# Kernel tuning notes

Measured on AMD Instinct MI355X. Metric: run time of the kernel, lower is better.

Reference implementation:

```python
import jax, jax.numpy as jnp
from jax import lax
import numpy as np
import math

B = 8
DIFF_LEN, HORIZON, NUM_NODES = 336, 96, 1024
SEG_LEN, D_CONV, D_MODEL = 8, 64, 128
NUM_KERNELS, DEPTH, ALPHA = 6, 2, 0.05
FREQ = math.ceil(DIFF_LEN / SEG_LEN)      # 42
STEP = math.ceil(HORIZON / SEG_LEN)       # 12
PAD = SEG_LEN * FREQ - DIFF_LEN           # 0 here, code stays general
MAXK = 2 * NUM_KERNELS - 1                # 11


def setup_inputs() -> dict:
    key = jax.random.key(0)
    ks = iter(jax.random.split(key, 64))
    p = lambda *s: 0.02 * jax.random.normal(next(ks), s, jnp.float32)
    inp = dict(
        x_diff=jax.random.normal(next(ks), (B, DIFF_LEN, NUM_NODES), jnp.float32),
        adj=jax.random.uniform(next(ks), (NUM_NODES, NUM_NODES), jnp.float32),
        enc_w1=p(SEG_LEN, D_MODEL), enc_b1=p(D_MODEL),
        enc_w2=p(D_MODEL, D_CONV), enc_b2=p(D_CONV),
        dec_w1=p(D_CONV, D_MODEL), dec_b1=p(D_MODEL),
        dec_w2=p(D_MODEL, SEG_LEN), dec_b2=p(SEG_LEN),
        g1_w=p((DEPTH + 1) * D_CONV, D_CONV), g1_b=p(D_CONV),
        g2_w=p((DEPTH + 1) * D_CONV, D_CONV), g2_b=p(D_CONV),
    )
    for i in range(NUM_KERNELS):
        inp[f'conv_w{i}'] = p(D_CONV, D_CONV, 1, 2 * i + 1)
        inp[f'conv_b{i}'] = p(D_CONV)
    return inp


def _mlp(x, w1, b1, w2, b2):
    # 2-hidden-layer MLP with ReLU (dropout = identity at eval)
    return jnp.maximum(x @ w1 + b1, 0.0) @ w2 + b2


def _t_inception(x, conv_ws, conv_bs):
    # x: (B, D, N, T); inception = mean of 'same'-padded (1, 2i+1) convs
    out = jnp.zeros_like(x)
    for i, (w, b) in enumerate(zip(conv_ws, conv_bs)):
        out = out + lax.conv_general_dilated(
            x, w, (1, 1), ((0, 0), (i, i)),
            dimension_numbers=('NCHW', 'OIHW', 'NCHW')) + b[None, :, None, None]
    return out / len(conv_ws)


def _norm_adj(adj):
    a = adj + jnp.eye(adj.shape[0], dtype=adj.dtype)
    return a / a.sum(1, keepdims=True)


def _mixprop(x, a, w, b):
    # x: (B, T, N, D), a: row-normalized (N, N)
    h = x
    outs = [h]
    for _ in range(DEPTH):
        h = ALPHA * x + (1.0 - ALPHA) * jnp.einsum('vn,btnd->btvd', a, h)
        outs.append(h)
    return jnp.concatenate(outs, -1) @ w + b


def _stconv(x, a1, a2, conv_ws, conv_bs, g1_w, g1_b, g2_w, g2_b):
    res = jnp.transpose(x, (0, 3, 2, 1))            # b d n t
    res = _t_inception(res, conv_ws, conv_bs)
    res = jnp.transpose(res, (0, 3, 2, 1))          # b t n d
    res = _mixprop(res, a1, g1_w, g1_b) + _mixprop(res, a2, g2_w, g2_b)
    return res + x                                   # dropout = identity at eval


def reference(x_diff, adj,
              enc_w1, enc_b1, enc_w2, enc_b2,
              dec_w1, dec_b1, dec_w2, dec_b2,
              g1_w, g1_b, g2_w, g2_b,
              conv_w0, conv_b0, conv_w1, conv_b1, conv_w2, conv_b2,
              conv_w3, conv_b3, conv_w4, conv_b4, conv_w5, conv_b5):
    conv_ws = [conv_w0, conv_w1, conv_w2, conv_w3, conv_w4, conv_w5]
    conv_bs = [conv_b0, conv_b1, conv_b2, conv_b3, conv_b4, conv_b5]
    Bb, L, N = x_diff.shape
    a1 = _norm_adj(adj)
    a2 = _norm_adj(adj.T)

    # segment + left-pad with tail so length = FREQ * SEG_LEN
    res = jnp.concatenate((x_diff[:, L - PAD:, :], x_diff), axis=1)
    res = res.reshape(Bb, FREQ, SEG_LEN, N)
    res = jnp.transpose(res, (0, 1, 3, 2))          # (B, F, N, P)
    res = _mlp(res, enc_w1, enc_b1, enc_w2, enc_b2)  # (B, F, N, D)

    # reconstruction branch (teacher-forced one-step shift)
    rec = jnp.concatenate(
        (res[:, :1],
         _stconv(res[:, :-1], a1, a2, conv_ws, conv_bs, g1_w, g1_b, g2_w, g2_b)),
        axis=1)
    rec = _mlp(rec, dec_w1, dec_b1, dec_w2, dec_b2)  # (B, F, N, P)
    rec = jnp.transpose(rec, (0, 1, 3, 2)).reshape(Bb, FREQ * SEG_LEN, N)
    rec = rec[:, -DIFF_LEN:, :]

    cur = res[:, -MAXK:]                             # (B, MAXK, N, D)
    preds = []
    for _ in range(STEP):
        p = _stconv(cur, a1, a2, conv_ws, conv_bs, g1_w, g1_b, g2_w, g2_b)[:, -1:]
        preds.append(p)
        cur = jnp.concatenate((cur[:, 1:], p), axis=1)
    pred = jnp.concatenate(preds, axis=1)            # (B, STEP, N, D)
    pred = _mlp(pred, dec_w1, dec_b1, dec_w2, dec_b2)  # (B, STEP, N, SEG)
    # NOTE: original torch code does a raw .reshape (not transpose); replicate it
    pred = pred.reshape(Bb, STEP * SEG_LEN, N)[:, :HORIZON, :]
    return (rec, pred)
```

## Files before the change

kernel.cpp:

```cpp
#include <hip/hip_runtime.h>

typedef __bf16 bf16;
typedef __bf16 bf16x8 __attribute__((ext_vector_type(8)));
typedef float f32x4 __attribute__((ext_vector_type(4)));

#define N_NODES 1024
#define DC 64
#define FREQ 42
#define TREC 41
#define NB 8
#define MAXK 11
#define NSTEP 12
#define SLICE 65536

__global__ void transpose_k(const float* __restrict__ in, float* __restrict__ out) {
  __shared__ float tile[32][33];
  int bx = blockIdx.x * 32, by = blockIdx.y * 32;
  int x = threadIdx.x, y = threadIdx.y;
#pragma unroll
  for (int j = 0; j < 32; j += 8) tile[y + j][x] = in[(size_t)(by + y + j) * N_NODES + bx + x];
  __syncthreads();
#pragma unroll
  for (int j = 0; j < 32; j += 8) out[(size_t)(bx + y + j) * N_NODES + by + x] = tile[x][y + j];
}

__global__ void rowsum_k(const float* __restrict__ m, float* __restrict__ sums) {
  int v = blockIdx.x;
  float s = 0.f;
  for (int n = threadIdx.x; n < N_NODES; n += 256) s += m[(size_t)v * N_NODES + n];
  __shared__ float red[256];
  red[threadIdx.x] = s;
  __syncthreads();
  for (int w = 128; w > 0; w >>= 1) {
    if (threadIdx.x < w) red[threadIdx.x] += red[threadIdx.x + w];
    __syncthreads();
  }
  if (threadIdx.x == 0) sums[v] = red[0] + 1.0f;
}

__global__ void norm_k(const float* __restrict__ adj, const float* __restrict__ adjT,
                       const float* __restrict__ rs, const float* __restrict__ cs,
                       bf16* __restrict__ a1, bf16* __restrict__ a2) {
  int v = blockIdx.x & (N_NODES - 1);
  bool second = blockIdx.x >= N_NODES;
  const float* src = second ? adjT : adj;
  float inv = 1.0f / (second ? cs[v] : rs[v]);
  bf16* dst = second ? a2 : a1;
  for (int n = threadIdx.x; n < N_NODES; n += 256) {
    float val = src[(size_t)v * N_NODES + n] + (n == v ? 1.0f : 0.0f);
    dst[(size_t)v * N_NODES + n] = (bf16)(val * inv);
  }
}

__global__ __launch_bounds__(256) void btrans_k(const bf16* __restrict__ src,
                                                bf16* __restrict__ dst) {
  __shared__ __align__(16) bf16 t[64][72];
  int bx = blockIdx.x * 64, by = blockIdx.y * 64;
  int tid = threadIdx.x;
#pragma unroll
  for (int i = 0; i < 2; ++i) {
    int q = tid + i * 256;
    int r = q >> 3, c = (q & 7) * 8;
    *(uint4*)&t[r][c] = *(const uint4*)&src[(size_t)(by + r) * N_NODES + bx + c];
  }
  __syncthreads();
#pragma unroll
  for (int i = 0; i < 2; ++i) {
    int q = tid + i * 256;
    int rr = q >> 3, cc = (q & 7) * 8;
    bf16 tmp[8];
#pragma unroll
    for (int e = 0; e < 8; ++e) tmp[e] = t[cc + e][rr];
    *(uint4*)&dst[(size_t)(bx + rr) * N_NODES + by + cc] = *(uint4*)tmp;
  }
}

__global__ void combine_w_k(const float* w0, const float* w1, const float* w2, const float* w3,
                            const float* w4, const float* w5, const float* b0, const float* b1,
                            const float* b2, const float* b3, const float* b4, const float* b5,
                            bf16* __restrict__ Wc, float* __restrict__ bsum) {
  int idx = blockIdx.x * 256 + threadIdx.x;
  if (idx < MAXK * 4096) {
    int dtI = idx >> 12;
    int dout = (idx >> 6) & 63;
    int di = idx & 63;
    int d = dtI - 5;
    int ad = d < 0 ? -d : d;
    const float* ws[6] = {w0, w1, w2, w3, w4, w5};
    float s = 0.f;
    for (int i = 0; i < 6; ++i)
      if (i >= ad) {
        int K = 2 * i + 1;
        s += ws[i][((size_t)dout * 64 + di) * K + (d + i)];
      }
    Wc[idx] = (bf16)s;
  }
  if (idx < 64) bsum[idx] = b0[idx] + b1[idx] + b2[idx] + b3[idx] + b4[idx] + b5[idx];
}

__global__ void vt_k(const float* __restrict__ g1w, const float* __restrict__ g2w,
                     const float* __restrict__ g1b, const float* __restrict__ g2b,
                     bf16* __restrict__ Vt, float* __restrict__ gbsum) {
  int idx = blockIdx.x * 256 + threadIdx.x;
  if (idx < 64) gbsum[idx] = g1b[idx] + g2b[idx];
  if (idx >= 5 * 4096) return;
  int j = idx >> 12;
  int dout = (idx >> 6) & 63;
  int din = idx & 63;
  const float al = 0.05f, bt = 0.95f;
  float v;
  if (j == 0)
    v = g1w[din * 64 + dout] + g2w[din * 64 + dout] +
        al * (g1w[(64 + din) * 64 + dout] + g1w[(128 + din) * 64 + dout] +
              g2w[(64 + din) * 64 + dout] + g2w[(128 + din) * 64 + dout]);
  else if (j == 1)
    v = bt * g1w[(64 + din) * 64 + dout] + al * bt * g1w[(128 + din) * 64 + dout];
  else if (j == 2)
    v = bt * bt * g1w[(128 + din) * 64 + dout];
  else if (j == 3)
    v = bt * g2w[(64 + din) * 64 + dout] + al * bt * g2w[(128 + din) * 64 + dout];
  else
    v = bt * bt * g2w[(128 + din) * 64 + dout];
  Vt[idx] = (bf16)v;
}

__global__ void prep_misc_k(const float* __restrict__ w2, const float* __restrict__ dw1,
                            const float* __restrict__ dw2, bf16* __restrict__ w2T,
                            bf16* __restrict__ dw1T, bf16* __restrict__ dw2T) {
  int i = blockIdx.x * 256 + threadIdx.x;
  if (i < 8192) {
    int dout = i >> 7, j = i & 127;
    w2T[i] = (bf16)w2[(size_t)j * 64 + dout];
    int jj = i >> 6, k = i & 63;
    dw1T[i] = (bf16)dw1[k * 128 + jj];
  }
  if (i < 2048) {
    int s = i >> 7, j = i & 127;
    dw2T[i] = (s < 8) ? (bf16)dw2[j * 8 + s] : (bf16)0.f;
  }
}

__global__ __launch_bounds__(256) void encoder_k(const float* __restrict__ x,
                                                 const float* __restrict__ w1,
                                                 const float* __restrict__ b1,
                                                 const bf16* __restrict__ w2T,
                                                 const float* __restrict__ b2,
                                                 bf16* __restrict__ resb) {
  __shared__ __align__(16) float xs[8 * 64];
  __shared__ __align__(16) float w1s[8 * 128];
  __shared__ float b1s[128];
  __shared__ float b2s[64];
  __shared__ __align__(16) bf16 hA[64 * 136];
  __shared__ __align__(16) bf16 wB[64 * 136];
  int tid = threadIdx.x;
  int v0 = blockIdx.x * 64;
  int bfp = blockIdx.y;
  int b = bfp / FREQ, f = bfp % FREQ;
#pragma unroll
  for (int i = 0; i < 2; ++i) {
    int q = tid + i * 256;
    xs[q] = x[(size_t)(b * 336 + f * 8 + (q >> 6)) * 1024 + v0 + (q & 63)];
  }
#pragma unroll
  for (int i = 0; i < 4; ++i) {
    int q = tid + i * 256;
    w1s[q] = w1[q];
  }
#pragma unroll
  for (int i = 0; i < 4; ++i) {
    int q = tid + i * 256;
    int dout = q >> 4, jc = (q & 15) * 8;
    *(uint4*)&wB[dout * 136 + jc] = *(const uint4*)&w2T[dout * 128 + jc];
  }
  if (tid < 128) b1s[tid] = b1[tid];
  if (tid < 64) b2s[tid] = b2[tid];
  __syncthreads();
  {
    int n = tid & 63, jc = (tid >> 6) * 32;
    for (int jj = 0; jj < 32; ++jj) {
      int j = jc + jj;
      float a = b1s[j];
#pragma unroll
      for (int k = 0; k < 8; ++k) a = fmaf(xs[k * 64 + n], w1s[k * 128 + j], a);
      hA[n * 136 + j] = (bf16)fmaxf(a, 0.f);
    }
  }
  __syncthreads();
  int wid = tid >> 6, lane = tid & 63, lr = lane & 15, lg = lane >> 4;
  f32x4 acc[4] = {};
#pragma unroll
  for (int ks = 0; ks < 4; ++ks) {
    bf16x8 a = *(const bf16x8*)&hA[(wid * 16 + lr) * 136 + ks * 32 + lg * 8];
#pragma unroll
    for (int ni = 0; ni < 4; ++ni) {
      bf16x8 bb = *(const bf16x8*)&wB[(ni * 16 + lr) * 136 + ks * 32 + lg * 8];
      acc[ni] = __builtin_amdgcn_mfma_f32_16x16x32_bf16(a, bb, acc[ni], 0, 0, 0);
    }
  }
  __syncthreads();
#pragma unroll
  for (int ni = 0; ni < 4; ++ni) {
    int n = ni * 16 + lr;
    float bz = b2s[n];
#pragma unroll
    for (int r = 0; r < 4; ++r) wB[(wid * 16 + lg * 4 + r) * 72 + n] = (bf16)(acc[ni][r] + bz);
  }
  __syncthreads();
  size_t so = (size_t)(b * FREQ + f) * SLICE;
#pragma unroll
  for (int i = 0; i < 2; ++i) {
    int q = tid + i * 256;
    int r = q >> 3, c = (q & 7) * 8;
    *(uint4*)&resb[so + (size_t)(v0 + r) * 64 + c] = *(uint4*)&wB[r * 72 + c];
  }
}

__global__ void curinit_k(const bf16* __restrict__ resb, float* __restrict__ cur,
                          bf16* __restrict__ curb) {
  size_t idx = (size_t)blockIdx.x * 256 + threadIdx.x;
  const size_t per_b = (size_t)MAXK * SLICE;
  if (idx < (size_t)NB * per_b) {
    size_t b = idx / per_b, rem = idx % per_b;
    bf16 v = resb[b * ((size_t)FREQ * SLICE) + (size_t)31 * SLICE + rem];
    cur[idx] = (float)v;
    curb[idx] = v;
  }
}

__device__ __forceinline__ void stageA(bf16* lds_a, const bf16* src, int rowStride, int tid) {
#pragma unroll
  for (int i = 0; i < 8; ++i) {
    int q = tid + i * 256;
    int r = q >> 3, c = (q & 7) << 3;
    *(uint4*)&lds_a[r * 72 + c] = *(const uint4*)&src[(size_t)r * rowStride + c];
  }
}
__device__ __forceinline__ void stageB(bf16* lds_b, const bf16* src, int rowStride, int tid) {
#pragma unroll
  for (int i = 0; i < 2; ++i) {
    int q = tid + i * 256;
    int r = q >> 3, c = (q & 7) << 3;
    *(uint4*)&lds_b[r * 72 + c] = *(const uint4*)&src[(size_t)r * rowStride + c];
  }
}
__device__ __forceinline__ void mfma64(const bf16* lds_a, const bf16* lds_b, int wid, int lane,
                                       f32x4 acc[4][4]) {
  int lr = lane & 15, lg = lane >> 4;
#pragma unroll
  for (int h = 0; h < 2; ++h) {
    bf16x8 af[4], bfr[4];
#pragma unroll
    for (int mi = 0; mi < 4; ++mi)
      af[mi] = *(const bf16x8*)&lds_a[(wid * 64 + mi * 16 + lr) * 72 + h * 32 + lg * 8];
#pragma unroll
    for (int ni = 0; ni < 4; ++ni)
      bfr[ni] = *(const bf16x8*)&lds_b[(ni * 16 + lr) * 72 + h * 32 + lg * 8];
#pragma unroll
    for (int mi = 0; mi < 4; ++mi)
#pragma unroll
      for (int ni = 0; ni < 4; ++ni)
        acc[mi][ni] =
            __builtin_amdgcn_mfma_f32_16x16x32_bf16(af[mi], bfr[ni], acc[mi][ni], 0, 0, 0);
  }
}

__global__ __launch_bounds__(256) void asq_k(const bf16* __restrict__ a,
                                             const bf16* __restrict__ aT,
                                             bf16* __restrict__ out) {
  __shared__ __align__(16) bf16 As[64 * 72];
  __shared__ __align__(16) bf16 Bs2[64 * 72];
  int tid = threadIdx.x, w = tid >> 6, lane = tid & 63;
  int lr = lane & 15, lg = lane >> 4;
  int v0 = blockIdx.x * 64, n0 = blockIdx.y * 64;
  f32x4 acc[4] = {};
  for (int k0 = 0; k0 < 1024; k0 += 64) {
    __syncthreads();
    stageB(As, a + (size_t)v0 * 1024 + k0, 1024, tid);
    stageB(Bs2, aT + (size_t)n0 * 1024 + k0, 1024, tid);
    __syncthreads();
#pragma unroll
    for (int h = 0; h < 2; ++h) {
      bf16x8 av = *(const bf16x8*)&As[(w * 16 + lr) * 72 + h * 32 + lg * 8];
#pragma unroll
      for (int ni = 0; ni < 4; ++ni) {
        bf16x8 bv = *(const bf16x8*)&Bs2[(ni * 16 + lr) * 72 + h * 32 + lg * 8];
        acc[ni] = __builtin_amdgcn_mfma_f32_16x16x32_bf16(av, bv, acc[ni], 0, 0, 0);
      }
    }
  }
#pragma unroll
  for (int ni = 0; ni < 4; ++ni)
#pragma unroll
    for (int r = 0; r < 4; ++r) As[(w * 16 + lg * 4 + r) * 72 + ni * 16 + lr] = (bf16)acc[ni][r];
  __syncthreads();
#pragma unroll
  for (int i = 0; i < 2; ++i) {
    int q = tid + i * 256;
    int r = q >> 3, c = (q & 7) * 8;
    *(uint4*)&out[(size_t)(v0 + r) * 1024 + n0 + c] = *(uint4*)&As[r * 72 + c];
  }
}

__global__ __launch_bounds__(256) void incep_k(const bf16* __restrict__ resb, int b0,
                                               const bf16* __restrict__ Wc,
                                               const float* __restrict__ bsum,
                                               bf16* __restrict__ xcN, bf16* __restrict__ xcF) {
  __shared__ __align__(16) bf16 lds_a[256 * 72];
  __shared__ __align__(16) bf16 lds_b[64 * 72];
  int tid = threadIdx.x, wid = tid >> 6, lane = tid & 63;
  int v0 = blockIdx.x * 256;
  int sl = blockIdx.y;
  int b = b0 + sl / TREC, tt = sl % TREC;
  f32x4 acc[4][4] = {};
  for (int dt = 0; dt < MAXK; ++dt) {
    int ts = tt + dt - 5;
    if (ts < 0 || ts >= TREC) continue;
    __syncthreads();
    stageA(lds_a, resb + (size_t)(b * FREQ + ts) * SLICE + (size_t)v0 * 64, 64, tid);
    stageB(lds_b, Wc + dt * 4096, 64, tid);
    __syncthreads();
    mfma64(lds_a, lds_b, wid, lane, acc);
  }
  int lr = lane & 15, lg = lane >> 4;
  size_t so = (size_t)sl * SLICE;
  __syncthreads();
#pragma unroll
  for (int mi = 0; mi < 4; ++mi)
#pragma unroll
    for (int ni = 0; ni < 4; ++ni) {
      int n = ni * 16 + lr;
      float bs = bsum[n];
      union { bf16 h[4]; uint2 u; } pk;
#pragma unroll
      for (int r = 0; r < 4; ++r) {
        int m = wid * 64 + mi * 16 + lg * 4 + r;
        bf16 bv = (bf16)((acc[mi][ni][r] + bs) * (1.f / 6.f));
        lds_a[m * 72 + n] = bv;
        pk.h[r] = bv;
      }
      *(uint2*)&xcF[so + (size_t)n * 1024 + v0 + wid * 64 + mi * 16 + lg * 4] = pk.u;
    }
  __syncthreads();
#pragma unroll
  for (int i = 0; i < 8; ++i) {
    int q = tid + i * 256;
    int r = q >> 3, c = (q & 7) * 8;
    *(uint4*)&xcN[so + (size_t)(v0 + r) * 64 + c] = *(uint4*)&lds_a[r * 72 + c];
  }
}

__global__ __launch_bounds__(256) void fusedrec_k(
    const bf16* __restrict__ xcN, const bf16* __restrict__ xcF, const bf16* __restrict__ a1,
    const bf16* __restrict__ a1q, const bf16* __restrict__ a2, const bf16* __restrict__ a2q,
    const bf16* __restrict__ Vt, const float* __restrict__ gbsum,
    const bf16* __restrict__ resb, int b0, const bf16* __restrict__ dw1T,
    const float* __restrict__ db1, const bf16* __restrict__ dw2T,
    const float* __restrict__ db2, float* __restrict__ outRec) {
  __shared__ __align__(16) bf16 reg1[4][64 * 72];
  __shared__ __align__(16) bf16 reg2[64 * 72];
  __shared__ __align__(16) bf16 valb[64 * 72];
  bf16* hb = &reg1[0][0];
  int tid = threadIdx.x, w = tid >> 6, lane = tid & 63;
  int lr = lane & 15, lg = lane >> 4;
  int v0 = blockIdx.x * 64;
  int sy = blockIdx.y;
  int bl = sy / FREQ, f = sy % FREQ;
  int b = b0 + bl;

  if (f == 0) {
    const bf16* src = resb + (size_t)(b * FREQ) * SLICE + (size_t)v0 * 64;
#pragma unroll
    for (int i = 0; i < 2; ++i) {
      int q = tid + i * 256;
      int r = q >> 3, c = (q & 7) * 8;
      *(uint4*)&valb[r * 72 + c] = *(const uint4*)&src[(size_t)r * 64 + c];
    }
    __syncthreads();
  } else {
    int tt = f - 1;
    size_t so = (size_t)(bl * TREC + tt) * SLICE;
    f32x4 acc[4][4] = {};
    for (int k0 = 0; k0 < 1024; k0 += 64) {
      __syncthreads();
#pragma unroll
      for (int i = 0; i < 8; ++i) {
        int q = tid + i * 256;
        int mm = q >> 9, pos = q & 511;
        int rr = pos >> 3, cc = (pos & 7) * 8;
        const bf16* mp = mm == 0 ? a1 : (mm == 1 ? a1q : (mm == 2 ? a2 : a2q));
        *(uint4*)&reg1[mm][rr * 72 + cc] = *(const uint4*)&mp[(size_t)(v0 + rr) * 1024 + k0 + cc];
      }
#pragma unroll
      for (int i = 0; i < 2; ++i) {
        int q = tid + i * 256;
        int rb = q >> 3, cbb = (q & 7) * 8;
        *(uint4*)&reg2[rb * 72 + cbb] = *(const uint4*)&xcF[so + (size_t)rb * 1024 + k0 + cbb];
      }
      __syncthreads();
#pragma unroll
      for (int h = 0; h < 2; ++h) {
        bf16x8 af[4], bfr[4];
#pragma unroll
        for (int mi = 0; mi < 4; ++mi)
          af[mi] = *(const bf16x8*)&reg1[w][(mi * 16 + lr) * 72 + h * 32 + lg * 8];
#pragma unroll
        for (int ni = 0; ni < 4; ++ni)
          bfr[ni] = *(const bf16x8*)&reg2[(ni * 16 + lr) * 72 + h * 32 + lg * 8];
#pragma unroll
        for (int mi = 0; mi < 4; ++mi)
#pragma unroll
          for (int ni = 0; ni < 4; ++ni)
            acc[mi][ni] =
                __builtin_amdgcn_mfma_f32_16x16x32_bf16(af[mi], bfr[ni], acc[mi][ni], 0, 0, 0);
      }
    }
    __syncthreads();
#pragma unroll
    for (int mi = 0; mi < 4; ++mi)
#pragma unroll
      for (int ni = 0; ni < 4; ++ni)
#pragma unroll
        for (int r = 0; r < 4; ++r)
          reg1[w][(mi * 16 + lg * 4 + r) * 72 + ni * 16 + lr] = (bf16)acc[mi][ni][r];
#pragma unroll
    for (int i = 0; i < 2; ++i) {
      int q = tid + i * 256;
      int r = q >> 3, c = (q & 7) * 8;
      *(uint4*)&reg2[r * 72 + c] = *(const uint4*)&xcN[so + (size_t)(v0 + r) * 64 + c];
    }
    __syncthreads();
    f32x4 z[4] = {};
#pragma unroll
    for (int j = 0; j < 5; ++j) {
      const bf16* Asrc = (j == 0) ? reg2 : &reg1[j - 1][0];
#pragma unroll
      for (int h = 0; h < 2; ++h) {
        bf16x8 a = *(const bf16x8*)&Asrc[(w * 16 + lr) * 72 + h * 32 + lg * 8];
#pragma unroll
        for (int ni = 0; ni < 4; ++ni) {
          bf16x8 bb =
              *(const bf16x8*)&Vt[(size_t)j * 4096 + (ni * 16 + lr) * 64 + h * 32 + lg * 8];
          z[ni] = __builtin_amdgcn_mfma_f32_16x16x32_bf16(a, bb, z[ni], 0, 0, 0);
        }
      }
    }
    const bf16* xb = resb + (size_t)(b * FREQ + tt) * SLICE + (size_t)v0 * 64;
#pragma unroll
    for (int ni = 0; ni < 4; ++ni) {
      int n = ni * 16 + lr;
      float gb = gbsum[n];
#pragma unroll
      for (int r = 0; r < 4; ++r) {
        int m = w * 16 + lg * 4 + r;
        valb[m * 72 + n] = (bf16)((float)xb[(size_t)m * 64 + n] + z[ni][r] + gb);
      }
    }
    __syncthreads();
  }
  f32x4 hacc[4][2] = {};
#pragma unroll
  for (int h = 0; h < 2; ++h) {
    bf16x8 a[4];
#pragma unroll
    for (int mi = 0; mi < 4; ++mi)
      a[mi] = *(const bf16x8*)&valb[(mi * 16 + lr) * 72 + h * 32 + lg * 8];
#pragma unroll
    for (int ni2 = 0; ni2 < 2; ++ni2) {
      bf16x8 bb = *(const bf16x8*)&dw1T[(w * 32 + ni2 * 16 + lr) * 64 + h * 32 + lg * 8];
#pragma unroll
      for (int mi = 0; mi < 4; ++mi)
        hacc[mi][ni2] = __builtin_amdgcn_mfma_f32_16x16x32_bf16(a[mi], bb, hacc[mi][ni2], 0, 0, 0);
    }
  }
  __syncthreads();
#pragma unroll
  for (int ni2 = 0; ni2 < 2; ++ni2) {
    int j = w * 32 + ni2 * 16 + lr;
    float bz = db1[j];
#pragma unroll
    for (int mi = 0; mi < 4; ++mi)
#pragma unroll
      for (int r = 0; r < 4; ++r)
        hb[(mi * 16 + lg * 4 + r) * 136 + j] = (bf16)fmaxf(hacc[mi][ni2][r] + bz, 0.f);
  }
  __syncthreads();
  f32x4 oacc = {};
#pragma unroll
  for (int kc = 0; kc < 4; ++kc) {
    bf16x8 a = *(const bf16x8*)&hb[(w * 16 + lr) * 136 + kc * 32 + lg * 8];
    bf16x8 bb = *(const bf16x8*)&dw2T[lr * 128 + kc * 32 + lg * 8];
    oacc = __builtin_amdgcn_mfma_f32_16x16x32_bf16(a, bb, oacc, 0, 0, 0);
  }
  if (lr < 8) {
    float bz = db2[lr];
    float4 o;
    o.x = oacc[0] + bz;
    o.y = oacc[1] + bz;
    o.z = oacc[2] + bz;
    o.w = oacc[3] + bz;
    *(float4*)&outRec[(size_t)b * 344064 + (size_t)(f * 8 + lr) * 1024 + v0 + w * 16 + lg * 4] =
        o;
  }
}

__device__ __forceinline__ void arrive_wait(unsigned* c, int tid) {
  __syncthreads();
  if (tid == 0) {
    __hip_atomic_fetch_add(c, 1u, __ATOMIC_RELAXED, __HIP_MEMORY_SCOPE_AGENT);
    while (__hip_atomic_load(c, __ATOMIC_RELAXED, __HIP_MEMORY_SCOPE_AGENT) < 64u)
      __builtin_amdgcn_s_sleep(8);
  }
  __syncthreads();
}

__device__ __forceinline__ void incep16(const bf16* __restrict__ curb,
                                        const bf16* __restrict__ Wc, const float* bsums_,
                                        int base, int b, int r0, int w, int lr, int lg,
                                        bf16* yL, bf16* yFdst) {
  f32x4 ya = {};
  for (int j = 0; j < 6; ++j) {
    int slot = (base + 5 + j) % MAXK;
    const bf16* cb = curb + ((size_t)b * MAXK + slot) * SLICE + (size_t)r0 * 64;
#pragma unroll
    for (int h = 0; h < 2; ++h) {
      bf16x8 a = *(const bf16x8*)&cb[lr * 64 + h * 32 + lg * 8];
      bf16x8 bb = *(const bf16x8*)&Wc[(size_t)j * 4096 + (w * 16 + lr) * 64 + h * 32 + lg * 8];
      ya = __builtin_amdgcn_mfma_f32_16x16x32_bf16(a, bb, ya, 0, 0, 0);
    }
  }
  int n = w * 16 + lr;
  float bs = bsums_[n];
  union { bf16 h[4]; unsigned long long u; } pk;
#pragma unroll
  for (int r = 0; r < 4; ++r) {
    int m = lg * 4 + r;
    bf16 bv = (bf16)((ya[r] + bs) * (1.f / 6.f));
    yL[m * 72 + n] = bv;
    pk.h[r] = bv;
  }
  __hip_atomic_store((unsigned long long*)(yFdst + (size_t)n * 1024 + r0 + lg * 4), pk.u,
                     __ATOMIC_RELAXED, __HIP_MEMORY_SCOPE_AGENT);
}

struct AR5 {
  const bf16 *Wc;
  const float *bsum;
  const bf16 *a1, *a1q, *a2, *a2q;
  const bf16 *Vt;
  const float *gbsum;
  float *cur;
  bf16 *curb;
  bf16 *yF;
  const bf16 *dw1T;
  const float *db1;
  const bf16 *dw2T;
  const float *db2;
  float *outPred;
  unsigned *bar;
};

__global__ void __launch_bounds__(256) ar6_k(AR5 p) {
  __shared__ __align__(16) bf16 As4[2][4][16 * 72];
  __shared__ __align__(16) bf16 Bs[2][64 * 72];
  __shared__ __align__(16) bf16 yL[16 * 72];
  __shared__ __align__(16) bf16 PL[4][16 * 72];
  __shared__ __align__(16) bf16 valb[16 * 72];
  __shared__ __align__(16) bf16 hb[16 * 136];
  __shared__ float db1s[128], db2s[8], bsums[64], gbsums[64];
  int tid = threadIdx.x, w = tid >> 6, lane = tid & 63;
  int lr = lane & 15, lg = lane >> 4;
  int bid = blockIdx.x, b = bid >> 6, l = bid & 63;
  unsigned* cnt = p.bar + b * 32;
  int r0 = l * 16;

  if (tid < 128) db1s[tid] = p.db1[tid];
  if (tid < 8) db2s[tid] = p.db2[tid];
  if (tid < 64) {
    bsums[tid] = p.bsum[tid];
    gbsums[tid] = p.gbsum[tid];
  }
  __syncthreads();

  incep16(p.curb, p.Wc, bsums, 0, b, r0, w, lr, lg, yL, p.yF + (size_t)b * SLICE);
  arrive_wait(cnt + 0, tid);

  const bf16* mats[4] = {p.a1, p.a1q, p.a2, p.a2q};
  for (int s = 0; s < NSTEP; ++s) {
    {
      const bf16* yFs = p.yF + ((size_t)s * NB + b) * SLICE;
      f32x4 acc[4] = {};
      auto stage_chunk = [&](int d, int k0) {
#pragma unroll
        for (int i = 0; i < 2; ++i) {
          int q = tid + i * 256;
          int mm = q >> 7, rr = (q >> 3) & 15, cc = (q & 7) * 8;
          *(uint4*)&As4[d][mm][rr * 72 + cc] =
              *(const uint4*)&mats[mm][(size_t)(r0 + rr) * 1024 + k0 + cc];
          int rb = q >> 3, cb2 = (q & 7) * 8;
          *(uint4*)&Bs[d][rb * 72 + cb2] = *(const uint4*)&yFs[(size_t)rb * 1024 + k0 + cb2];
        }
      };
      stage_chunk(0, 0);
      for (int c = 0; c < 16; ++c) {
        __syncthreads();
        if (c < 15) stage_chunk((c + 1) & 1, (c + 1) * 64);
#pragma unroll
        for (int h = 0; h < 2; ++h) {
          bf16x8 a = *(const bf16x8*)&As4[c & 1][w][lr * 72 + h * 32 + lg * 8];
#pragma unroll
          for (int ni = 0; ni < 4; ++ni) {
            bf16x8 bb = *(const bf16x8*)&Bs[c & 1][(ni * 16 + lr) * 72 + h * 32 + lg * 8];
            acc[ni] = __builtin_amdgcn_mfma_f32_16x16x32_bf16(a, bb, acc[ni], 0, 0, 0);
          }
        }
      }
#pragma unroll
      for (int ni = 0; ni < 4; ++ni) {
        int nn = ni * 16 + lr;
#pragma unroll
        for (int r = 0; r < 4; ++r) PL[w][(lg * 4 + r) * 72 + nn] = (bf16)acc[ni][r];
      }
    }
    __syncthreads();
    {
      f32x4 z = {};
#pragma unroll
      for (int j = 0; j < 5; ++j) {
        const bf16* Aj = (j == 0) ? yL : PL[j - 1];
#pragma unroll
        for (int h = 0; h < 2; ++h) {
          bf16x8 a = *(const bf16x8*)&Aj[lr * 72 + h * 32 + lg * 8];
          bf16x8 bb =
              *(const bf16x8*)&p.Vt[(size_t)j * 4096 + (w * 16 + lr) * 64 + h * 32 + lg * 8];
          z = __builtin_amdgcn_mfma_f32_16x16x32_bf16(a, bb, z, 0, 0, 0);
        }
      }
      int slotR = (s + 10) % MAXK, slotW = s % MAXK;
      size_t xo = ((size_t)b * MAXK + slotR) * SLICE + (size_t)r0 * 64;
      size_t wo = ((size_t)b * MAXK + slotW) * SLICE + (size_t)r0 * 64;
      int n = w * 16 + lr;
      float gb = gbsums[n];
#pragma unroll
      for (int r = 0; r < 4; ++r) {
        int m = lg * 4 + r;
        size_t o = (size_t)m * 64 + n;
        float v = p.cur[xo + o] + z[r] + gb;
        p.cur[wo + o] = v;
        p.curb[wo + o] = (bf16)v;
        valb[m * 72 + n] = (bf16)v;
      }
      __syncthreads();
      if (s < NSTEP - 1)
        incep16(p.curb, p.Wc, bsums, s + 1, b, r0, w, lr, lg, yL,
                p.yF + ((size_t)(s + 1) * NB + b) * SLICE);
      f32x4 hacc[2] = {};
#pragma unroll
      for (int h = 0; h < 2; ++h) {
        bf16x8 a = *(const bf16x8*)&valb[lr * 72 + h * 32 + lg * 8];
#pragma unroll
        for (int ni2 = 0; ni2 < 2; ++ni2) {
          bf16x8 bb = *(const bf16x8*)&p.dw1T[(w * 32 + ni2 * 16 + lr) * 64 + h * 32 + lg * 8];
          hacc[ni2] = __builtin_amdgcn_mfma_f32_16x16x32_bf16(a, bb, hacc[ni2], 0, 0, 0);
        }
      }
#pragma unroll
      for (int ni2 = 0; ni2 < 2; ++ni2) {
        int j = w * 32 + ni2 * 16 + lr;
        float bz = db1s[j];
#pragma unroll
        for (int r = 0; r < 4; ++r)
          hb[(lg * 4 + r) * 136 + j] = (bf16)fmaxf(hacc[ni2][r] + bz, 0.f);
      }
      __syncthreads();
      f32x4 oacc = {};
#pragma unroll
      for (int kc = 0; kc < 4; ++kc) {
        bf16x8 a = *(const bf16x8*)&hb[lr * 136 + kc * 32 + lg * 8];
        bf16x8 bb = *(const bf16x8*)&p.dw2T[lr * 128 + kc * 32 + lg * 8];
        oacc = __builtin_amdgcn_mfma_f32_16x16x32_bf16(a, bb, oacc, 0, 0, 0);
      }
      if (w == 0 && lr < 8) {
        float bz = db2s[lr];
#pragma unroll
        for (int r = 0; r < 4; ++r)
          p.outPred[(size_t)b * 98304 + (size_t)s * 8192 + (size_t)(r0 + lg * 4 + r) * 8 + lr] =
              oacc[r] + bz;
      }
    }
    if (s < NSTEP - 1) arrive_wait(cnt + 1 + s, tid);
  }
}

extern "C" void kernel_launch(void* const* d_in, const int* in_sizes, int n_in, void* d_out,
                              int out_size, void* d_ws, size_t ws_size, hipStream_t stream) {
  const float* x_diff = (const float*)d_in[0];
  const float* adj = (const float*)d_in[1];
  const float* enc_w1 = (const float*)d_in[2];
  const float* enc_b1 = (const float*)d_in[3];
  const float* enc_w2 = (const float*)d_in[4];
  const float* enc_b2 = (const float*)d_in[5];
  const float* dec_w1 = (const float*)d_in[6];
  const float* dec_b1 = (const float*)d_in[7];
  const float* dec_w2 = (const float*)d_in[8];
  const float* dec_b2 = (const float*)d_in[9];
  const float* g1_w = (const float*)d_in[10];
  const float* g1_b = (const float*)d_in[11];
  const float* g2_w = (const float*)d_in[12];
  const float* g2_b = (const float*)d_in[13];
  const float* cw[6];
  const float* cb_[6];
  for (int i = 0; i < 6; ++i) {
    cw[i] = (const float*)d_in[14 + 2 * i];
    cb_[i] = (const float*)d_in[15 + 2 * i];
  }

  char* base = (char*)d_ws;
  size_t off = 0;
  auto alloc = [&](size_t bytes) -> void* {
    void* p = base + off;
    off = (off + bytes + 255) & ~(size_t)255;
    return p;
  };
  float* adjT = (float*)alloc(1048576ULL * 4);
  float* rowsum = (float*)alloc(4096);
  float* colsum = (float*)alloc(4096);
  bf16* a1b = (bf16*)alloc(1048576ULL * 2);
  bf16* a2b = (bf16*)alloc(1048576ULL * 2);
  bf16* a1T = (bf16*)alloc(1048576ULL * 2);
  bf16* a2T = (bf16*)alloc(1048576ULL * 2);
  bf16* a1q = (bf16*)alloc(1048576ULL * 2);
  bf16* a2q = (bf16*)alloc(1048576ULL * 2);
  bf16* Wc = (bf16*)alloc(45056ULL * 2);
  float* bsum = (float*)alloc(256);
  float* gbsum = (float*)alloc(256);
  bf16* Vt = (bf16*)alloc(20480ULL * 2);
  bf16* w2T = (bf16*)alloc(8192ULL * 2);
  bf16* dw1T = (bf16*)alloc(8192ULL * 2);
  bf16* dw2T = (bf16*)alloc(2048ULL * 2);
  bf16* resb = (bf16*)alloc((size_t)NB * FREQ * SLICE * 2);
  float* cur = (float*)alloc((size_t)NB * MAXK * SLICE * 4);
  bf16* curb = (bf16*)alloc((size_t)NB * MAXK * SLICE * 2);
  bf16* yF = (bf16*)alloc((size_t)NSTEP * NB * SLICE * 2);
  unsigned* gbar = (unsigned*)alloc(4096);
  size_t fixedEnd = off;
  int cb = NB;
  while (cb > 1) {
    size_t S = (size_t)TREC * cb;
    if (fixedEnd + S * SLICE * 4 + 65536 <= ws_size) break;
    cb >>= 1;
  }
  size_t S = (size_t)TREC * cb;
  bf16* xcN = (bf16*)alloc(S * SLICE * 2);
  bf16* xcF = (bf16*)alloc(S * SLICE * 2);

  float* outF = (float*)d_out;
  float* outRec = outF;
  float* outPred = outF + (size_t)2752512;

  transpose_k<<<dim3(32, 32), dim3(32, 8), 0, stream>>>(adj, adjT);
  rowsum_k<<<1024, 256, 0, stream>>>(adj, rowsum);
  rowsum_k<<<1024, 256, 0, stream>>>(adjT, colsum);
  norm_k<<<2048, 256, 0, stream>>>(adj, adjT, rowsum, colsum, a1b, a2b);
  btrans_k<<<dim3(16, 16), 256, 0, stream>>>(a1b, a1T);
  btrans_k<<<dim3(16, 16), 256, 0, stream>>>(a2b, a2T);
  asq_k<<<dim3(16, 16), 256, 0, stream>>>(a1b, a1T, a1q);
  asq_k<<<dim3(16, 16), 256, 0, stream>>>(a2b, a2T, a2q);
  combine_w_k<<<(MAXK * 4096 + 255) / 256, 256, 0, stream>>>(cw[0], cw[1], cw[2], cw[3], cw[4],
                                                             cw[5], cb_[0], cb_[1], cb_[2],
                                                             cb_[3], cb_[4], cb_[5], Wc, bsum);
  vt_k<<<80, 256, 0, stream>>>(g1_w, g2_w, g1_b, g2_b, Vt, gbsum);
  prep_misc_k<<<32, 256, 0, stream>>>(enc_w2, dec_w1, dec_w2, w2T, dw1T, dw2T);
  encoder_k<<<dim3(16, NB * FREQ), 256, 0, stream>>>(x_diff, enc_w1, enc_b1, w2T, enc_b2,
                                                     resb);
  curinit_k<<<(int)(((size_t)NB * MAXK * SLICE + 255) / 256), 256, 0, stream>>>(resb, cur,
                                                                                curb);

  for (int c0 = 0; c0 < NB; c0 += cb) {
    int Sg = TREC * cb;
    incep_k<<<dim3(4, Sg), 256, 0, stream>>>(resb, c0, Wc, bsum, xcN, xcF);
    fusedrec_k<<<dim3(16, cb * FREQ), 256, 0, stream>>>(xcN, xcF, a1b, a1q, a2b, a2q, Vt,
                                                        gbsum, resb, c0, dw1T, dec_b1, dw2T,
                                                        dec_b2, outRec);
  }

  hipMemsetAsync(gbar, 0, 4096, stream);
  AR5 arp;
  arp.Wc = Wc; arp.bsum = bsum;
  arp.a1 = a1b; arp.a1q = a1q; arp.a2 = a2b; arp.a2q = a2q;
  arp.Vt = Vt; arp.gbsum = gbsum;
  arp.cur = cur; arp.curb = curb;
  arp.yF = yF;
  arp.dw1T = dw1T; arp.db1 = dec_b1; arp.dw2T = dw2T; arp.db2 = dec_b2;
  arp.outPred = outPred;
  arp.bar = gbar;
  ar6_k<<<dim3(512), dim3(256), 0, stream>>>(arp);
}
```

Baseline: 827.1 us.

## Process two batch slices per block in fused reconstruction kernel to reuse adjacency tiles

Each block of the fused reconstruction kernel now computes two batch elements at once. The four adjacency-matrix tiles loaded into shared memory are reused for both slices' graph-propagation GEMMs, which halves adjacency traffic and halves the grid size. The cost is roughly double the accumulator registers and more shared memory per block, which lowers occupancy and may cause register spills.

```diff
diff --git a/kernel.cpp b/kernel.cpp
--- a/kernel.cpp
+++ b/kernel.cpp
@@ -349,37 +349,54 @@
   }
 }
 
-__global__ __launch_bounds__(256) void fusedrec_k(
+__global__ __launch_bounds__(256) void fusedrec2_k(
     const bf16* __restrict__ xcN, const bf16* __restrict__ xcF, const bf16* __restrict__ a1,
     const bf16* __restrict__ a1q, const bf16* __restrict__ a2, const bf16* __restrict__ a2q,
     const bf16* __restrict__ Vt, const float* __restrict__ gbsum,
-    const bf16* __restrict__ resb, int b0, const bf16* __restrict__ dw1T,
+    const bf16* __restrict__ resb, int b0, int cbN, const bf16* __restrict__ dw1T,
     const float* __restrict__ db1, const bf16* __restrict__ dw2T,
     const float* __restrict__ db2, float* __restrict__ outRec) {
-  __shared__ __align__(16) bf16 reg1[4][64 * 72];
-  __shared__ __align__(16) bf16 reg2[64 * 72];
-  __shared__ __align__(16) bf16 valb[64 * 72];
-  bf16* hb = &reg1[0][0];
+  __shared__ __align__(16) bf16 regA[4][64 * 72];
+  __shared__ __align__(16) bf16 regB1[64 * 72];
+  __shared__ __align__(16) bf16 regB2[64 * 72];
+  __shared__ __align__(16) bf16 valb1[64 * 72];
+  __shared__ __align__(16) bf16 valb2[64 * 72];
+  bf16* hb1 = &regA[0][0];
+  bf16* hb2 = hb1 + 64 * 136;
   int tid = threadIdx.x, w = tid >> 6, lane = tid & 63;
   int lr = lane & 15, lg = lane >> 4;
   int v0 = blockIdx.x * 64;
   int sy = blockIdx.y;
-  int bl = sy / FREQ, f = sy % FREQ;
-  int b = b0 + bl;
+  int half = (cbN + 1) >> 1;
+  int bp = sy / FREQ, f = sy % FREQ;
+  int bl1 = bp, bl2 = bp + half;
+  bool has2 = bl2 < cbN;
+  int b1 = b0 + bl1, b2 = b0 + bl2;
 
   if (f == 0) {
-    const bf16* src = resb + (size_t)(b * FREQ) * SLICE + (size_t)v0 * 64;
+    const bf16* src1 = resb + (size_t)(b1 * FREQ) * SLICE + (size_t)v0 * 64;
 #pragma unroll
     for (int i = 0; i < 2; ++i) {
       int q = tid + i * 256;
       int r = q >> 3, c = (q & 7) * 8;
-      *(uint4*)&valb[r * 72 + c] = *(const uint4*)&src[(size_t)r * 64 + c];
+      *(uint4*)&valb1[r * 72 + c] = *(const uint4*)&src1[(size_t)r * 64 + c];
+    }
+    if (has2) {
+      const bf16* src2 = resb + (size_t)(b2 * FREQ) * SLICE + (size_t)v0 * 64;
+#pragma unroll
+      for (int i = 0; i < 2; ++i) {
+        int q = tid + i * 256;
+        int r = q >> 3, c = (q & 7) * 8;
+        *(uint4*)&valb2[r * 72 + c] = *(const uint4*)&src2[(size_t)r * 64 + c];
+      }
     }
     __syncthreads();
   } else {
     int tt = f - 1;
-    size_t so = (size_t)(bl * TREC + tt) * SLICE;
-    f32x4 acc[4][4] = {};
+    size_t so1 = (size_t)(bl1 * TREC + tt) * SLICE;
+    size_t so2 = (size_t)(bl2 * TREC + tt) * SLICE;
+    f32x4 acc1[4][4] = {};
+    f32x4 acc2[4][4] = {};
     for (int k0 = 0; k0 < 1024; k0 += 64) {
       __syncthreads();
 #pragma unroll
@@ -388,30 +405,46 @@
         int mm = q >> 9, pos = q & 511;
         int rr = pos >> 3, cc = (pos & 7) * 8;
         const bf16* mp = mm == 0 ? a1 : (mm == 1 ? a1q : (mm == 2 ? a2 : a2q));
-        *(uint4*)&reg1[mm][rr * 72 + cc] = *(const uint4*)&mp[(size_t)(v0 + rr) * 1024 + k0 + cc];
+        *(uint4*)&regA[mm][rr * 72 + cc] =
+            *(const uint4*)&mp[(size_t)(v0 + rr) * 1024 + k0 + cc];
       }
 #pragma unroll
       for (int i = 0; i < 2; ++i) {
         int q = tid + i * 256;
         int rb = q >> 3, cbb = (q & 7) * 8;
-        *(uint4*)&reg2[rb * 72 + cbb] = *(const uint4*)&xcF[so + (size_t)rb * 1024 + k0 + cbb];
+        *(uint4*)&regB1[rb * 72 + cbb] = *(const uint4*)&xcF[so1 + (size_t)rb * 1024 + k0 + cbb];
+      }
+      if (has2) {
+#pragma unroll
+        for (int i = 0; i < 2; ++i) {
+          int q = tid + i * 256;
+          int rb = q >> 3, cbb = (q & 7) * 8;
+          *(uint4*)&regB2[rb * 72 + cbb] =
+              *(const uint4*)&xcF[so2 + (size_t)rb * 1024 + k0 + cbb];
+        }
       }
       __syncthreads();
 #pragma unroll
       for (int h = 0; h < 2; ++h) {
-        bf16x8 af[4], bfr[4];
+        bf16x8 af[4];
 #pragma unroll
         for (int mi = 0; mi < 4; ++mi)
-          af[mi] = *(const bf16x8*)&reg1[w][(mi * 16 + lr) * 72 + h * 32 + lg * 8];
-#pragma unroll
-        for (int ni = 0; ni < 4; ++ni)
-          bfr[ni] = *(const bf16x8*)&reg2[(ni * 16 + lr) * 72 + h * 32 + lg * 8];
-#pragma unroll
-        for (int mi = 0; mi < 4; ++mi)
-#pragma unroll
-          for (int ni = 0; ni < 4; ++ni)
-            acc[mi][ni] =
-                __builtin_amdgcn_mfma_f32_16x16x32_bf16(af[mi], bfr[ni], acc[mi][ni], 0, 0, 0);
+          af[mi] = *(const bf16x8*)&regA[w][(mi * 16 + lr) * 72 + h * 32 + lg * 8];
+#pragma unroll
+        for (int ni = 0; ni < 4; ++ni) {
+          bf16x8 bf1 = *(const bf16x8*)&regB1[(ni * 16 + lr) * 72 + h * 32 + lg * 8];
+#pragma unroll
+          for (int mi = 0; mi < 4; ++mi)
+            acc1[mi][ni] =
+                __builtin_amdgcn_mfma_f32_16x16x32_bf16(af[mi], bf1, acc1[mi][ni], 0, 0, 0);
+          if (has2) {
+            bf16x8 bf2 = *(const bf16x8*)&regB2[(ni * 16 + lr) * 72 + h * 32 + lg * 8];
+#pragma unroll
+            for (int mi = 0; mi < 4; ++mi)
+              acc2[mi][ni] =
+                  __builtin_amdgcn_mfma_f32_16x16x32_bf16(af[mi], bf2, acc2[mi][ni], 0, 0, 0);
+          }
+        }
       }
     }
     __syncthreads();
@@ -421,55 +454,105 @@
       for (int ni = 0; ni < 4; ++ni)
 #pragma unroll
         for (int r = 0; r < 4; ++r)
-          reg1[w][(mi * 16 + lg * 4 + r) * 72 + ni * 16 + lr] = (bf16)acc[mi][ni][r];
+          regA[w][(mi * 16 + lg * 4 + r) * 72 + ni * 16 + lr] = (bf16)acc1[mi][ni][r];
 #pragma unroll
     for (int i = 0; i < 2; ++i) {
       int q = tid + i * 256;
       int r = q >> 3, c = (q & 7) * 8;
-      *(uint4*)&reg2[r * 72 + c] = *(const uint4*)&xcN[so + (size_t)(v0 + r) * 64 + c];
-    }
-    __syncthreads();
-    f32x4 z[4] = {};
-#pragma unroll
-    for (int j = 0; j < 5; ++j) {
-      const bf16* Asrc = (j == 0) ? reg2 : &reg1[j - 1][0];
-#pragma unroll
-      for (int h = 0; h < 2; ++h) {
-        bf16x8 a = *(const bf16x8*)&Asrc[(w * 16 + lr) * 72 + h * 32 + lg * 8];
-#pragma unroll
-        for (int ni = 0; ni < 4; ++ni) {
-          bf16x8 bb =
-              *(const bf16x8*)&Vt[(size_t)j * 4096 + (ni * 16 + lr) * 64 + h * 32 + lg * 8];
-          z[ni] = __builtin_amdgcn_mfma_f32_16x16x32_bf16(a, bb, z[ni], 0, 0, 0);
-        }
-      }
-    }
-    const bf16* xb = resb + (size_t)(b * FREQ + tt) * SLICE + (size_t)v0 * 64;
-#pragma unroll
-    for (int ni = 0; ni < 4; ++ni) {
-      int n = ni * 16 + lr;
-      float gb = gbsum[n];
-#pragma unroll
-      for (int r = 0; r < 4; ++r) {
-        int m = w * 16 + lg * 4 + r;
-        valb[m * 72 + n] = (bf16)((float)xb[(size_t)m * 64 + n] + z[ni][r] + gb);
-      }
-    }
-    __syncthreads();
-  }
-  f32x4 hacc[4][2] = {};
+      *(uint4*)&regB1[r * 72 + c] = *(const uint4*)&xcN[so1 + (size_t)(v0 + r) * 64 + c];
+    }
+    __syncthreads();
+    {
+      f32x4 z[4] = {};
+#pragma unroll
+      for (int j = 0; j < 5; ++j) {
+        const bf16* Asrc = (j == 0) ? regB1 : &regA[j - 1][0];
+#pragma unroll
+        for (int h = 0; h < 2; ++h) {
+          bf16x8 a = *(const bf16x8*)&Asrc[(w * 16 + lr) * 72 + h * 32 + lg * 8];
+#pragma unroll
+          for (int ni = 0; ni < 4; ++ni) {
+            bf16x8 bb =
+                *(const bf16x8*)&Vt[(size_t)j * 4096 + (ni * 16 + lr) * 64 + h * 32 + lg * 8];
+            z[ni] = __builtin_amdgcn_mfma_f32_16x16x32_bf16(a, bb, z[ni], 0, 0, 0);
+          }
+        }
+      }
+      const bf16* xb = resb + (size_t)(b1 * FREQ + tt) * SLICE + (size_t)v0 * 64;
+#pragma unroll
+      for (int ni = 0; ni < 4; ++ni) {
+        int n = ni * 16 + lr;
+        float gb = gbsum[n];
+#pragma unroll
+        for (int r = 0; r < 4; ++r) {
+          int m = w * 16 + lg * 4 + r;
+          valb1[m * 72 + n] = (bf16)((float)xb[(size_t)m * 64 + n] + z[ni][r] + gb);
+        }
+      }
+    }
+    __syncthreads();
+    if (has2) {
+#pragma unroll
+      for (int mi = 0; mi < 4; ++mi)
+#pragma unroll
+        for (int ni = 0; ni < 4; ++ni)
+#pragma unroll
+          for (int r = 0; r < 4; ++r)
+            regA[w][(mi * 16 + lg * 4 + r) * 72 + ni * 16 + lr] = (bf16)acc2[mi][ni][r];
+#pragma unroll
+      for (int i = 0; i < 2; ++i) {
+        int q = tid + i * 256;
+        int r = q >> 3, c = (q & 7) * 8;
+        *(uint4*)&regB2[r * 72 + c] = *(const uint4*)&xcN[so2 + (size_t)(v0 + r) * 64 + c];
+      }
+      __syncthreads();
+      f32x4 z[4] = {};
+#pragma unroll
+      for (int j = 0; j < 5; ++j) {
+        const bf16* Asrc = (j == 0) ? regB2 : &regA[j - 1][0];
+#pragma unroll
+        for (int h = 0; h < 2; ++h) {
+          bf16x8 a = *(const bf16x8*)&Asrc[(w * 16 + lr) * 72 + h * 32 + lg * 8];
+#pragma unroll
+          for (int ni = 0; ni < 4; ++ni) {
+            bf16x8 bb =
+                *(const bf16x8*)&Vt[(size_t)j * 4096 + (ni * 16 + lr) * 64 + h * 32 + lg * 8];
+            z[ni] = __builtin_amdgcn_mfma_f32_16x16x32_bf16(a, bb, z[ni], 0, 0, 0);
+          }
+        }
+      }
+      const bf16* xb = resb + (size_t)(b2 * FREQ + tt) * SLICE + (size_t)v0 * 64;
+#pragma unroll
+      for (int ni = 0; ni < 4; ++ni) {
+        int n = ni * 16 + lr;
+        float gb = gbsum[n];
+#pragma unroll
+        for (int r = 0; r < 4; ++r) {
+          int m = w * 16 + lg * 4 + r;
+          valb2[m * 72 + n] = (bf16)((float)xb[(size_t)m * 64 + n] + z[ni][r] + gb);
+        }
+      }
+      __syncthreads();
+    }
+  }
+  f32x4 hacc1[4][2] = {};
+  f32x4 hacc2[4][2] = {};
 #pragma unroll
   for (int h = 0; h < 2; ++h) {
-    bf16x8 a[4];
-#pragma unroll
-    for (int mi = 0; mi < 4; ++mi)
-      a[mi] = *(const bf16x8*)&valb[(mi * 16 + lr) * 72 + h * 32 + lg * 8];
 #pragma unroll
     for (int ni2 = 0; ni2 < 2; ++ni2) {
       bf16x8 bb = *(const bf16x8*)&dw1T[(w * 32 + ni2 * 16 + lr) * 64 + h * 32 + lg * 8];
 #pragma unroll
-      for (int mi = 0; mi < 4; ++mi)
-        hacc[mi][ni2] = __builtin_amdgcn_mfma_f32_16x16x32_bf16(a[mi], bb, hacc[mi][ni2], 0, 0, 0);
+      for (int mi = 0; mi < 4; ++mi) {
+        bf16x8 a1v = *(const bf16x8*)&valb1[(mi * 16 + lr) * 72 + h * 32 + lg * 8];
+        hacc1[mi][ni2] =
+            __builtin_amdgcn_mfma_f32_16x16x32_bf16(a1v, bb, hacc1[mi][ni2], 0, 0, 0);
+        if (has2) {
+          bf16x8 a2v = *(const bf16x8*)&valb2[(mi * 16 + lr) * 72 + h * 32 + lg * 8];
+          hacc2[mi][ni2] =
+              __builtin_amdgcn_mfma_f32_16x16x32_bf16(a2v, bb, hacc2[mi][ni2], 0, 0, 0);
+        }
+      }
     }
   }
   __syncthreads();
@@ -480,26 +563,43 @@
 #pragma unroll
     for (int mi = 0; mi < 4; ++mi)
 #pragma unroll
-      for (int r = 0; r < 4; ++r)
-        hb[(mi * 16 + lg * 4 + r) * 136 + j] = (bf16)fmaxf(hacc[mi][ni2][r] + bz, 0.f);
-  }
-  __syncthreads();
-  f32x4 oacc = {};
+      for (int r = 0; r < 4; ++r) {
+        int m = mi * 16 + lg * 4 + r;
+        hb1[m * 136 + j] = (bf16)fmaxf(hacc1[mi][ni2][r] + bz, 0.f);
+        if (has2) hb2[m * 136 + j] = (bf16)fmaxf(hacc2[mi][ni2][r] + bz, 0.f);
+      }
+  }
+  __syncthreads();
+  f32x4 oacc1 = {};
+  f32x4 oacc2 = {};
 #pragma unroll
   for (int kc = 0; kc < 4; ++kc) {
-    bf16x8 a = *(const bf16x8*)&hb[(w * 16 + lr) * 136 + kc * 32 + lg * 8];
     bf16x8 bb = *(const bf16x8*)&dw2T[lr * 128 + kc * 32 + lg * 8];
-    oacc = __builtin_amdgcn_mfma_f32_16x16x32_bf16(a, bb, oacc, 0, 0, 0);
+    bf16x8 a1v = *(const bf16x8*)&hb1[(w * 16 + lr) * 136 + kc * 32 + lg * 8];
+    oacc1 = __builtin_amdgcn_mfma_f32_16x16x32_bf16(a1v, bb, oacc1, 0, 0, 0);
+    if (has2) {
+      bf16x8 a2v = *(const bf16x8*)&hb2[(w * 16 + lr) * 136 + kc * 32 + lg * 8];
+      oacc2 = __builtin_amdgcn_mfma_f32_16x16x32_bf16(a2v, bb, oacc2, 0, 0, 0);
+    }
   }
   if (lr < 8) {
     float bz = db2[lr];
     float4 o;
-    o.x = oacc[0] + bz;
-    o.y = oacc[1] + bz;
-    o.z = oacc[2] + bz;
-    o.w = oacc[3] + bz;
-    *(float4*)&outRec[(size_t)b * 344064 + (size_t)(f * 8 + lr) * 1024 + v0 + w * 16 + lg * 4] =
-        o;
+    o.x = oacc1[0] + bz;
+    o.y = oacc1[1] + bz;
+    o.z = oacc1[2] + bz;
+    o.w = oacc1[3] + bz;
+    *(float4*)&outRec[(size_t)b1 * 344064 + (size_t)(f * 8 + lr) * 1024 + v0 + w * 16 +
+                      lg * 4] = o;
+    if (has2) {
+      float4 o2;
+      o2.x = oacc2[0] + bz;
+      o2.y = oacc2[1] + bz;
+      o2.z = oacc2[2] + bz;
+      o2.w = oacc2[3] + bz;
+      *(float4*)&outRec[(size_t)b2 * 344064 + (size_t)(f * 8 + lr) * 1024 + v0 + w * 16 +
+                        lg * 4] = o2;
+    }
   }
 }
 
@@ -778,9 +878,10 @@
   for (int c0 = 0; c0 < NB; c0 += cb) {
     int Sg = TREC * cb;
     incep_k<<<dim3(4, Sg), 256, 0, stream>>>(resb, c0, Wc, bsum, xcN, xcF);
-    fusedrec_k<<<dim3(16, cb * FREQ), 256, 0, stream>>>(xcN, xcF, a1b, a1q, a2b, a2q, Vt,
-                                                        gbsum, resb, c0, dw1T, dec_b1, dw2T,
-                                                        dec_b2, outRec);
+    int half = (cb + 1) >> 1;
+    fusedrec2_k<<<dim3(16, half * FREQ), 256, 0, stream>>>(xcN, xcF, a1b, a1q, a2b, a2q, Vt,
+                                                           gbsum, resb, c0, cb, dw1T, dec_b1,
+                                                           dw2T, dec_b2, outRec);
   }
 
   hipMemsetAsync(gbar, 0, 4096, stream);
```

Result: slower. 1.010 ms (+22.1%).
